# Kernel tuning notes

Measured on AMD Instinct MI355X. Metric: run time of the kernel, lower is better.

The kernel has to match this reference:

```python
import jax, jax.numpy as jnp
import numpy as np
from jax import lax

EPS = 1e-5
B = 512

def _conv(x, w, pad):
    # x: [B,Cin,H,W], w: [Cout,Cin,kh,kw]
    return lax.conv_general_dilated(x, w, (1, 1), [(pad, pad), (pad, pad)],
                                    dimension_numbers=('NCHW', 'OIHW', 'NCHW'))

def _bn2d(x, g, b, m, v):
    s = g * lax.rsqrt(v + EPS)
    return x * s[None, :, None, None] + (b - m * s)[None, :, None, None]

def _bn1d(x, g, b, m, v):
    s = g * lax.rsqrt(v + EPS)
    return x * s + (b - m * s)

def _pool2(x):
    return lax.reduce_window(x, -jnp.inf, lax.max, (1, 1, 2, 2), (1, 1, 2, 2), 'VALID')

def setup_inputs() -> dict:
    key = jax.random.key(0)
    ks = iter(jax.random.split(key, 64))
    rn = lambda shape, s=1.0: jax.random.normal(next(ks), shape, dtype=jnp.float32) * s
    un = lambda shape: jax.random.uniform(next(ks), shape, dtype=jnp.float32, minval=0.5, maxval=1.5)
    def bn_params(c):
        return (jnp.ones((c,), jnp.float32), jnp.zeros((c,), jnp.float32), rn((c,), 0.1), un((c,)))
    inp = {"x": rn((B, 3, 64, 64))}
    inp["w1"] = rn((32, 3, 5, 5), 0.1)
    inp["bn1_g"], inp["bn1_b"], inp["bn1_m"], inp["bn1_v"] = bn_params(32)
    inp["w2"] = rn((64, 32, 3, 3), 0.06)
    inp["bn2_g"], inp["bn2_b"], inp["bn2_m"], inp["bn2_v"] = bn_params(64)
    inp["w3"] = rn((128, 64, 3, 3), 0.04)
    inp["bn3_g"], inp["bn3_b"], inp["bn3_m"], inp["bn3_v"] = bn_params(128)
    inp["fc_w"] = rn((256, 8192), 0.01)
    inp["fc_b"] = jnp.zeros((256,), jnp.float32)
    inp["bnf_g"], inp["bnf_b"], inp["bnf_m"], inp["bnf_v"] = bn_params(256)
    inp["c_w1"] = rn((64, 256), 0.06)
    inp["c_b1"] = jnp.zeros((64,), jnp.float32)
    inp["bnc_g"], inp["bnc_b"], inp["bnc_m"], inp["bnc_v"] = bn_params(64)
    inp["c_w2"] = rn((1, 64), 0.1)
    inp["c_b2"] = jnp.zeros((1,), jnp.float32)
    inp["m_w1"] = rn((64, 256), 0.06)
    inp["m_b1"] = jnp.zeros((64,), jnp.float32)
    inp["bnm_g"], inp["bnm_b"], inp["bnm_m"], inp["bnm_v"] = bn_params(64)
    inp["m_w2"] = rn((1, 64), 0.1)
    inp["m_b2"] = jnp.zeros((1,), jnp.float32)
    return inp

def reference(x, w1, bn1_g, bn1_b, bn1_m, bn1_v,
              w2, bn2_g, bn2_b, bn2_m, bn2_v,
              w3, bn3_g, bn3_b, bn3_m, bn3_v,
              fc_w, fc_b, bnf_g, bnf_b, bnf_m, bnf_v,
              c_w1, c_b1, bnc_g, bnc_b, bnc_m, bnc_v, c_w2, c_b2,
              m_w1, m_b1, bnm_g, bnm_b, bnm_m, bnm_v, m_w2, m_b2):
    # Block 1: conv5x5(3->32) + BN + ReLU + maxpool2 -> [B,32,32,32]
    h = _pool2(jax.nn.relu(_bn2d(_conv(x, w1, 2), bn1_g, bn1_b, bn1_m, bn1_v)))
    # Block 2: conv3x3(32->64) + BN + ReLU + maxpool2 -> [B,64,16,16]
    h = _pool2(jax.nn.relu(_bn2d(_conv(h, w2, 1), bn2_g, bn2_b, bn2_m, bn2_v)))
    # Block 3: conv3x3(64->128) + BN + ReLU + maxpool2 + ToDense -> [B,128,8,8]
    h = _pool2(jax.nn.relu(_bn2d(_conv(h, w3, 1), bn3_g, bn3_b, bn3_m, bn3_v)))
    f = h.reshape(h.shape[0], -1)  # [B, 8192]
    s = jax.nn.relu(_bn1d(f @ fc_w.T + fc_b, bnf_g, bnf_b, bnf_m, bnf_v))  # [B,256]
    c = jax.nn.relu(_bn1d(s @ c_w1.T + c_b1, bnc_g, bnc_b, bnc_m, bnc_v)) @ c_w2.T + c_b2
    mo = jax.nn.relu(_bn1d(s @ m_w1.T + m_b1, bnm_g, bnm_b, bnm_m, bnm_v)) @ m_w2.T + m_b2
    return (c, mo)  # ([B,1], [B,1])
```

## Files before the change

### kernel.cpp

```cpp
#include <hip/hip_runtime.h>
#include <hip/hip_bf16.h>

#define EPS 1e-5f

typedef __attribute__((ext_vector_type(8))) short bf16x8;
typedef __attribute__((ext_vector_type(4))) float f32x4;

__device__ __forceinline__ ushort f2b(float f) {
    return __builtin_bit_cast(ushort, __float2bfloat16(f));
}
__device__ __forceinline__ bf16x8 ld_frag(const void* p) {
    return __builtin_bit_cast(bf16x8, *reinterpret_cast<const uint4*>(p));
}

__global__ __launch_bounds__(256) void k_prep_all(
    const float* __restrict__ w1, const float* __restrict__ w2,
    const float* __restrict__ w3, const float* __restrict__ fcw,
    const float* __restrict__ x,
    ushort* __restrict__ w1p, ushort* __restrict__ w2p, ushort* __restrict__ w3p,
    ushort* __restrict__ fcwp, ushort* __restrict__ x4p,
    ushort* __restrict__ h1p, ushort* __restrict__ h2p)
{
    __shared__ ushort l[128 * 66];
    const int bid = blockIdx.x, t = threadIdx.x;
    if (bid < 128) {
        const int total = 5120 + 18432 + 73728;
        for (int i = bid * 256 + t; i < total; i += 128 * 256) {
            if (i < 5120) {
                const int ky = i >> 10, co = (i >> 5) & 31, k = i & 31;
                const int kx = k >> 2, ci = k & 3;
                float v = 0.f;
                if (kx < 5 && ci < 3) v = w1[((co * 3 + ci) * 5 + ky) * 5 + kx];
                w1p[i] = f2b(v);
            } else if (i < 5120 + 18432) {
                const int j = i - 5120;
                const int tap = j >> 11, co = (j >> 5) & 63, ci = j & 31;
                w2p[j] = f2b(w2[(co * 32 + ci) * 9 + tap]);
            } else {
                const int j = i - (5120 + 18432);
                const int tap = j >> 13, co = (j >> 6) & 127, ci = j & 63;
                w3p[j] = f2b(w3[(co * 64 + ci) * 9 + tap]);
            }
        }
    } else if (bid < 384) {
        const int j = bid - 128;
        const float* src = fcw + (size_t)j * 8192;
        #pragma unroll
        for (int i = 0; i < 32; ++i) {
            const int idx = i * 256 + t;
            const int c = idx >> 6, p = idx & 63;
            l[c * 66 + p] = f2b(src[idx]);
        }
        __syncthreads();
        ushort* dst = fcwp + (size_t)j * 8192;
        #pragma unroll
        for (int i = 0; i < 32; ++i) {
            const int idx = i * 256 + t;
            const int c = idx & 127, p = idx >> 7;
            dst[idx] = l[c * 66 + p];
        }
    } else if (bid < 4480) {
        for (int p = (bid - 384) * 256 + t; p < 2506752; p += 4096 * 256) {
            const int n = p / 4896;
            const int rem = p - n * 4896;
            const int row = rem / 72, col = rem - row * 72;
            const int gr = row - 2, gc = col - 2;
            ushort4 pk; pk.x = 0; pk.y = 0; pk.z = 0; pk.w = 0;
            if ((unsigned)gr < 64u && (unsigned)gc < 64u) {
                const size_t base = ((size_t)n * 3 << 12) + (gr << 6) + gc;
                pk.x = f2b(x[base]); pk.y = f2b(x[base + 4096]); pk.z = f2b(x[base + 8192]);
            }
            *reinterpret_cast<ushort4*>(&x4p[(size_t)p * 4]) = pk;
        }
    } else if (bid < 4736) {
        const uint4 z = {0, 0, 0, 0};
        for (int i = (bid - 4480) * 256 + t; i < 270336; i += 256 * 256) {
            const int img = i / 528;
            const int rem = i - img * 528;
            const int px = rem >> 2, gg = rem & 3;
            int row, col;
            if (px < 34)      { row = 0;  col = px; }
            else if (px < 68) { row = 33; col = px - 34; }
            else { const int q = px - 68; row = 1 + (q >> 1); col = (q & 1) ? 33 : 0; }
            *reinterpret_cast<uint4*>(&h1p[(((size_t)img * 34 + row) * 34 + col) * 32 + gg * 8]) = z;
        }
    } else if (bid < 4992) {
        const uint4 z = {0, 0, 0, 0};
        for (int i = (bid - 4736) * 256 + t; i < 278528; i += 256 * 256) {
            const int img = i / 544;
            const int rem = i - img * 544;
            const int px = rem >> 3, gg = rem & 7;
            int row, col;
            if (px < 18)      { row = 0;  col = px; }
            else if (px < 36) { row = 17; col = px - 18; }
            else { const int q = px - 36; row = 1 + (q >> 1); col = (q & 1) ? 17 : 0; }
            *reinterpret_cast<uint4*>(&h2p[(((size_t)img * 18 + row) * 18 + col) * 64 + gg * 8]) = z;
        }
    }
}

__global__ __launch_bounds__(256) void k_conv1(
    const ushort* __restrict__ x4p, const ushort* __restrict__ w1p,
    const float* __restrict__ bg, const float* __restrict__ bb,
    const float* __restrict__ bm, const float* __restrict__ bv,
    ushort* __restrict__ h1p)
{
    __shared__ __align__(16) ushort xs[12 * 72 * 4];
    __shared__ __align__(16) ushort ws[5 * 32 * 32];
    const int bid = blockIdx.x;
    const int n = bid >> 3, q = bid & 7;
    const int t = threadIdx.x;
    const int wave = t >> 6, lane = t & 63;
    const int g = lane >> 4, l15 = lane & 15;

    {
        const ushort* src = x4p + ((size_t)(n * 68 + 8 * q) * 72) * 4;
        for (int i = t; i < 432; i += 256)
            *reinterpret_cast<uint4*>(&xs[i * 8]) = *reinterpret_cast<const uint4*>(src + i * 8);
    }
    for (int i = t; i < 640; i += 256) {
        const int gg = i & 3, r = i >> 2;
        const int co = r & 31;
        const uint4 v = *reinterpret_cast<const uint4*>(&w1p[r * 32 + gg * 8]);
        *reinterpret_cast<uint4*>((char*)ws + r * 64 + ((gg ^ ((co >> 1) & 3)) << 4)) = v;
    }
    __syncthreads();

    f32x4 acc[8][2];
    #pragma unroll
    for (int i = 0; i < 8; ++i) { acc[i][0] = (f32x4){0,0,0,0}; acc[i][1] = (f32x4){0,0,0,0}; }

    const char* xsb = (const char*)xs;
    const char* wsb = (const char*)ws;
    #pragma unroll
    for (int ky = 0; ky < 5; ++ky) {
        bf16x8 a[8], b[2];
        #pragma unroll
        for (int mt = 0; mt < 8; ++mt) {
            const int crl = 2 * wave + (mt >> 2);
            const int ccl = (mt & 3) * 16 + l15;
            const int off = ((crl + ky) * 72 + ccl) * 8 + g * 16;
            const uint2 lo = *reinterpret_cast<const uint2*>(xsb + off);
            const uint2 hi = *reinterpret_cast<const uint2*>(xsb + off + 8);
            uint4 all; all.x = lo.x; all.y = lo.y; all.z = hi.x; all.w = hi.y;
            a[mt] = __builtin_bit_cast(bf16x8, all);
        }
        #pragma unroll
        for (int nt = 0; nt < 2; ++nt) {
            const int co = nt * 16 + l15;
            b[nt] = ld_frag(wsb + (ky * 32 + co) * 64 + ((g ^ ((co >> 1) & 3)) << 4));
        }
        #pragma unroll
        for (int mt = 0; mt < 8; ++mt)
            #pragma unroll
            for (int nt = 0; nt < 2; ++nt)
                acc[mt][nt] = __builtin_amdgcn_mfma_f32_16x16x32_bf16(a[mt], b[nt], acc[mt][nt], 0, 0, 0);
    }

    const int prow = q * 4 + wave;
    #pragma unroll
    for (int nt = 0; nt < 2; ++nt) {
        const int co = nt * 16 + l15;
        const float s = bg[co] * rsqrtf(bv[co] + EPS);
        const float bsv = bb[co] - bm[co] * s;
        #pragma unroll
        for (int mt = 0; mt < 4; ++mt) {
            #pragma unroll
            for (int j = 0; j < 2; ++j) {
                const float v0 = fmaxf(fmaf(acc[mt][nt][2 * j],     s, bsv), 0.f);
                const float v1 = fmaxf(fmaf(acc[mt][nt][2 * j + 1], s, bsv), 0.f);
                const float v2 = fmaxf(fmaf(acc[mt + 4][nt][2 * j],     s, bsv), 0.f);
                const float v3 = fmaxf(fmaf(acc[mt + 4][nt][2 * j + 1], s, bsv), 0.f);
                const int ppc = mt * 8 + g * 2 + j;
                h1p[(((size_t)n * 34 + prow + 1) * 34 + ppc + 1) * 32 + co] =
                    f2b(fmaxf(fmaxf(v0, v1), fmaxf(v2, v3)));
            }
        }
    }
}

__global__ __launch_bounds__(256) void k_conv2(
    const ushort* __restrict__ h1p, const ushort* __restrict__ w2p,
    const float* __restrict__ bg, const float* __restrict__ bb,
    const float* __restrict__ bm, const float* __restrict__ bv,
    ushort* __restrict__ h2p)
{
    __shared__ __align__(16) ushort xs[10 * 34 * 32];
    __shared__ __align__(16) ushort ws[9 * 64 * 32];
    const int bid = blockIdx.x;
    const int n = bid >> 2, q = bid & 3;
    const int t = threadIdx.x;
    const int wave = t >> 6, lane = t & 63;
    const int g = lane >> 4, l15 = lane & 15;
    const char* xsb = (const char*)xs;
    const char* wsb = (const char*)ws;

    for (int i = t; i < 2304; i += 256) {
        const int gg = i & 3, r = i >> 2;
        const int co = r & 63;
        const uint4 v = *reinterpret_cast<const uint4*>(&w2p[r * 32 + gg * 8]);
        *reinterpret_cast<uint4*>((char*)ws + r * 64 + ((gg ^ ((co >> 1) & 3)) << 4)) = v;
    }
    {
        const ushort* src = h1p + ((size_t)(n * 34 + 8 * q) * 34) * 32;
        for (int i = t; i < 1360; i += 256) {
            const int gg = i & 3, pix = i >> 2;
            const uint4 v = *reinterpret_cast<const uint4*>(src + i * 8);
            *reinterpret_cast<uint4*>((char*)xs + pix * 64 + ((gg ^ ((pix >> 1) & 3)) << 4)) = v;
        }
    }
    __syncthreads();

    f32x4 acc[4][4];
    #pragma unroll
    for (int i = 0; i < 4; ++i)
        #pragma unroll
        for (int j = 0; j < 4; ++j) acc[i][j] = (f32x4){0,0,0,0};

    #pragma unroll
    for (int tap = 0; tap < 9; ++tap) {
        const int ky = tap / 3, kx = tap - 3 * ky;
        bf16x8 a[4], b[4];
        #pragma unroll
        for (int mt = 0; mt < 4; ++mt) {
            const int crl = 2 * wave + (mt >> 1);
            const int ccl = (mt & 1) * 16 + l15;
            const int pix = (crl + ky) * 34 + ccl + kx;
            a[mt] = ld_frag(xsb + pix * 64 + ((g ^ ((pix >> 1) & 3)) << 4));
        }
        #pragma unroll
        for (int nt = 0; nt < 4; ++nt) {
            const int co = nt * 16 + l15;
            b[nt] = ld_frag(wsb + (tap * 64 + co) * 64 + ((g ^ ((co >> 1) & 3)) << 4));
        }
        #pragma unroll
        for (int mt = 0; mt < 4; ++mt)
            #pragma unroll
            for (int nt = 0; nt < 4; ++nt)
                acc[mt][nt] = __builtin_amdgcn_mfma_f32_16x16x32_bf16(a[mt], b[nt], acc[mt][nt], 0, 0, 0);
    }

    const int prow = q * 4 + wave;
    #pragma unroll
    for (int nt = 0; nt < 4; ++nt) {
        const int co = nt * 16 + l15;
        const float s = bg[co] * rsqrtf(bv[co] + EPS);
        const float bsv = bb[co] - bm[co] * s;
        #pragma unroll
        for (int mtl = 0; mtl < 2; ++mtl) {
            #pragma unroll
            for (int j = 0; j < 2; ++j) {
                const float v0 = fmaxf(fmaf(acc[mtl][nt][2 * j],     s, bsv), 0.f);
                const float v1 = fmaxf(fmaf(acc[mtl][nt][2 * j + 1], s, bsv), 0.f);
                const float v2 = fmaxf(fmaf(acc[mtl + 2][nt][2 * j],     s, bsv), 0.f);
                const float v3 = fmaxf(fmaf(acc[mtl + 2][nt][2 * j + 1], s, bsv), 0.f);
                const int ppc = mtl * 8 + g * 2 + j;
                h2p[(((size_t)n * 18 + prow + 1) * 18 + ppc + 1) * 64 + co] =
                    f2b(fmaxf(fmaxf(v0, v1), fmaxf(v2, v3)));
            }
        }
    }
}

__global__ __launch_bounds__(256) void k_conv3(
    const ushort* __restrict__ h2p, const ushort* __restrict__ w3p,
    const float* __restrict__ bg, const float* __restrict__ bb,
    const float* __restrict__ bm, const float* __restrict__ bv,
    ushort* __restrict__ h3)
{
    __shared__ __align__(16) ushort xs[324 * 32];
    __shared__ __align__(16) ushort ws[9 * 64 * 32];
    const int bid = blockIdx.x;
    const int n = bid >> 1, ch = bid & 1;
    const int t = threadIdx.x;
    const int wave = t >> 6, lane = t & 63;
    const int g = lane >> 4, l15 = lane & 15;
    const char* xsb = (const char*)xs;
    const char* wsb = (const char*)ws;

    f32x4 acc[4][4];
    #pragma unroll
    for (int i = 0; i < 4; ++i)
        #pragma unroll
        for (int j = 0; j < 4; ++j) acc[i][j] = (f32x4){0,0,0,0};

    for (int gci = 0; gci < 2; ++gci) {
        if (gci) __syncthreads();
        for (int i = t; i < 1296; i += 256) {
            const int gg = i & 3, pix = i >> 2;
            const uint4 v = *reinterpret_cast<const uint4*>(
                &h2p[((size_t)n * 324 + pix) * 64 + gci * 32 + gg * 8]);
            *reinterpret_cast<uint4*>((char*)xs + pix * 64 + ((gg ^ ((pix >> 1) & 3)) << 4)) = v;
        }
        for (int i = t; i < 2304; i += 256) {
            const int gg = i & 3, r = i >> 2;
            const int tap = r >> 6, co = r & 63;
            const uint4 v = *reinterpret_cast<const uint4*>(
                &w3p[((size_t)(tap * 128 + ch * 64 + co) << 6) + gci * 32 + gg * 8]);
            *reinterpret_cast<uint4*>((char*)ws + r * 64 + ((gg ^ ((co >> 1) & 3)) << 4)) = v;
        }
        __syncthreads();
        #pragma unroll
        for (int tap = 0; tap < 9; ++tap) {
            const int ky = tap / 3, kx = tap - 3 * ky;
            bf16x8 a[4], b[4];
            #pragma unroll
            for (int mt = 0; mt < 4; ++mt) {
                const int pr = 4 * wave + mt;
                const int pix = (pr + ky) * 18 + l15 + kx;
                a[mt] = ld_frag(xsb + pix * 64 + ((g ^ ((pix >> 1) & 3)) << 4));
            }
            #pragma unroll
            for (int nt = 0; nt < 4; ++nt) {
                const int co = nt * 16 + l15;
                b[nt] = ld_frag(wsb + (tap * 64 + co) * 64 + ((g ^ ((co >> 1) & 3)) << 4));
            }
            #pragma unroll
            for (int mt = 0; mt < 4; ++mt)
                #pragma unroll
                for (int nt = 0; nt < 4; ++nt)
                    acc[mt][nt] = __builtin_amdgcn_mfma_f32_16x16x32_bf16(a[mt], b[nt], acc[mt][nt], 0, 0, 0);
        }
    }

    #pragma unroll
    for (int nt = 0; nt < 4; ++nt) {
        const int co = ch * 64 + nt * 16 + l15;
        const float s = bg[co] * rsqrtf(bv[co] + EPS);
        const float bsv = bb[co] - bm[co] * s;
        #pragma unroll
        for (int mtl = 0; mtl < 2; ++mtl) {
            #pragma unroll
            for (int j = 0; j < 2; ++j) {
                const int mt = mtl * 2;
                const float v0 = fmaxf(fmaf(acc[mt][nt][2 * j],     s, bsv), 0.f);
                const float v1 = fmaxf(fmaf(acc[mt][nt][2 * j + 1], s, bsv), 0.f);
                const float v2 = fmaxf(fmaf(acc[mt + 1][nt][2 * j],     s, bsv), 0.f);
                const float v3 = fmaxf(fmaf(acc[mt + 1][nt][2 * j + 1], s, bsv), 0.f);
                const int ppr = 2 * wave + mtl;
                const int pcol = g * 2 + j;
                h3[(((size_t)n * 8 + ppr) * 8 + pcol) * 128 + co] =
                    f2b(fmaxf(fmaxf(v0, v1), fmaxf(v2, v3)));
            }
        }
    }
}

__global__ __launch_bounds__(256) void k_fc(
    const ushort* __restrict__ A, const ushort* __restrict__ Bw, float* __restrict__ C)
{
    __shared__ __align__(16) ushort As[64 * 32];
    __shared__ __align__(16) ushort Bs[64 * 32];
    const int bm = blockIdx.x, bn = blockIdx.y, kz = blockIdx.z;
    const int t = threadIdx.x;
    const int wave = t >> 6, lane = t & 63;
    const int g = lane >> 4, l15 = lane & 15;

    f32x4 acc[4];
    #pragma unroll
    for (int i = 0; i < 4; ++i) acc[i] = (f32x4){0,0,0,0};

    const char* asb = (const char*)As;
    const char* bsb = (const char*)Bs;
    for (int kk = 0; kk < 16; ++kk) {
        const int k0 = kz * 512 + kk * 32;
        if (kk) __syncthreads();
        {
            const int gg = t & 3, row = t >> 2;
            const uint4 va = *reinterpret_cast<const uint4*>(
                &A[(size_t)(bm * 64 + row) * 8192 + k0 + gg * 8]);
            *reinterpret_cast<uint4*>((char*)As + row * 64 + ((gg ^ ((row >> 1) & 3)) << 4)) = va;
            const uint4 vb = *reinterpret_cast<const uint4*>(
                &Bw[(size_t)(bn * 64 + row) * 8192 + k0 + gg * 8]);
            *reinterpret_cast<uint4*>((char*)Bs + row * 64 + ((gg ^ ((row >> 1) & 3)) << 4)) = vb;
        }
        __syncthreads();
        bf16x8 a[4], b;
        #pragma unroll
        for (int mt = 0; mt < 4; ++mt) {
            const int r = mt * 16 + l15;
            a[mt] = ld_frag(asb + r * 64 + ((g ^ ((r >> 1) & 3)) << 4));
        }
        {
            const int r = wave * 16 + l15;
            b = ld_frag(bsb + r * 64 + ((g ^ ((r >> 1) & 3)) << 4));
        }
        #pragma unroll
        for (int mt = 0; mt < 4; ++mt)
            acc[mt] = __builtin_amdgcn_mfma_f32_16x16x32_bf16(a[mt], b, acc[mt], 0, 0, 0);
    }

    float* Cp = C + (size_t)kz * 512 * 256;
    const int col = bn * 64 + wave * 16 + l15;
    #pragma unroll
    for (int mt = 0; mt < 4; ++mt) {
        #pragma unroll
        for (int r = 0; r < 4; ++r) {
            const int row = bm * 64 + mt * 16 + g * 4 + r;
            Cp[(size_t)row * 256 + col] = acc[mt][r];
        }
    }
}

__global__ __launch_bounds__(128) void k_heads(
    const float* __restrict__ sraw, const float* __restrict__ fcb,
    const float* __restrict__ fg, const float* __restrict__ fb,
    const float* __restrict__ fm, const float* __restrict__ fv,
    const float* __restrict__ cw1, const float* __restrict__ cb1,
    const float* __restrict__ cg, const float* __restrict__ cbb,
    const float* __restrict__ cm, const float* __restrict__ cv,
    const float* __restrict__ cw2, const float* __restrict__ cb2,
    const float* __restrict__ mw1, const float* __restrict__ mb1,
    const float* __restrict__ mg, const float* __restrict__ mbb,
    const float* __restrict__ mm, const float* __restrict__ mv,
    const float* __restrict__ mw2, const float* __restrict__ mb2,
    float* __restrict__ outp)
{
    __shared__ float sv[256];
    const int b = blockIdx.x, t = threadIdx.x;
    for (int k = t; k < 256; k += 128) {
        float val = fcb[k];
        #pragma unroll
        for (int z = 0; z < 16; ++z) val += sraw[(size_t)z * 131072 + b * 256 + k];
        const float s = fg[k] * rsqrtf(fv[k] + EPS);
        sv[k] = fmaxf(fmaf(val, s, fb[k] - fm[k] * s), 0.f);
    }
    __syncthreads();
    const int j = t & 63;
    const bool isM = (t >= 64);
    const float* w1  = isM ? mw1 : cw1;
    const float* b1  = isM ? mb1 : cb1;
    const float* g1  = isM ? mg  : cg;
    const float* bb1 = isM ? mbb : cbb;
    const float* m1  = isM ? mm  : cm;
    const float* v1  = isM ? mv  : cv;
    const float* w2  = isM ? mw2 : cw2;
    const float* b2  = isM ? mb2 : cb2;
    float d = 0.f;
    const float* wr = w1 + j * 256;
    #pragma unroll 8
    for (int k = 0; k < 256; ++k) d = fmaf(sv[k], wr[k], d);
    d += b1[j];
    const float s1 = g1[j] * rsqrtf(v1[j] + EPS);
    d = fmaxf(fmaf(d, s1, bb1[j] - m1[j] * s1), 0.f);
    float prod = d * w2[j];
    #pragma unroll
    for (int off = 32; off > 0; off >>= 1) prod += __shfl_down(prod, off);
    if (j == 0) outp[(isM ? 512 : 0) + b] = prod + b2[0];
}

extern "C" void kernel_launch(void* const* d_in, const int* in_sizes, int n_in,
                              void* d_out, int out_size, void* d_ws, size_t ws_size,
                              hipStream_t stream)
{
    const float* x    = (const float*)d_in[0];
    const float* w1   = (const float*)d_in[1];
    const float* bn1g = (const float*)d_in[2];
    const float* bn1b = (const float*)d_in[3];
    const float* bn1m = (const float*)d_in[4];
    const float* bn1v = (const float*)d_in[5];
    const float* w2   = (const float*)d_in[6];
    const float* bn2g = (const float*)d_in[7];
    const float* bn2b = (const float*)d_in[8];
    const float* bn2m = (const float*)d_in[9];
    const float* bn2v = (const float*)d_in[10];
    const float* w3   = (const float*)d_in[11];
    const float* bn3g = (const float*)d_in[12];
    const float* bn3b = (const float*)d_in[13];
    const float* bn3m = (const float*)d_in[14];
    const float* bn3v = (const float*)d_in[15];
    const float* fcw  = (const float*)d_in[16];
    const float* fcb  = (const float*)d_in[17];
    const float* bnfg = (const float*)d_in[18];
    const float* bnfb = (const float*)d_in[19];
    const float* bnfm = (const float*)d_in[20];
    const float* bnfv = (const float*)d_in[21];
    const float* cw1  = (const float*)d_in[22];
    const float* cb1  = (const float*)d_in[23];
    const float* bncg = (const float*)d_in[24];
    const float* bncb = (const float*)d_in[25];
    const float* bncm = (const float*)d_in[26];
    const float* bncv = (const float*)d_in[27];
    const float* cw2  = (const float*)d_in[28];
    const float* cb2  = (const float*)d_in[29];
    const float* mw1  = (const float*)d_in[30];
    const float* mb1  = (const float*)d_in[31];
    const float* bnmg = (const float*)d_in[32];
    const float* bnmb = (const float*)d_in[33];
    const float* bnmm = (const float*)d_in[34];
    const float* bnmv = (const float*)d_in[35];
    const float* mw2  = (const float*)d_in[36];
    const float* mb2  = (const float*)d_in[37];

    char* W = (char*)d_ws;
    ushort* x4p  = (ushort*)(W);
    ushort* h1p  = (ushort*)(W + 20054016);
    ushort* h2p  = (ushort*)(W + 57933824);
    ushort* h3   = (ushort*)(W + 79167488);
    ushort* w1p  = (ushort*)(W + 87556096);
    ushort* w2p  = (ushort*)(W + 87566336);
    ushort* w3p  = (ushort*)(W + 87603200);
    ushort* fcwp = (ushort*)(W + 87750656);
    float*  sr   = (float*) (W + 91944960);
    float* outp = (float*)d_out;

    k_prep_all<<<4992, 256, 0, stream>>>(w1, w2, w3, fcw, x,
                                         w1p, w2p, w3p, fcwp, x4p, h1p, h2p);
    k_conv1<<<512 * 8, 256, 0, stream>>>(x4p, w1p, bn1g, bn1b, bn1m, bn1v, h1p);
    k_conv2<<<512 * 4, 256, 0, stream>>>(h1p, w2p, bn2g, bn2b, bn2m, bn2v, h2p);
    k_conv3<<<512 * 2, 256, 0, stream>>>(h2p, w3p, bn3g, bn3b, bn3m, bn3v, h3);
    k_fc<<<dim3(8, 4, 16), 256, 0, stream>>>(h3, fcwp, sr);
    k_heads<<<512, 128, 0, stream>>>(sr, fcb, bnfg, bnfb, bnfm, bnfv,
                                     cw1, cb1, bncg, bncb, bncm, bncv, cw2, cb2,
                                     mw1, mb1, bnmg, bnmb, bnmm, bnmv, mw2, mb2, outp);
}
```

Baseline: 250.0 us.

## Fold BN scale into conv weights and read weights from global instead of LDS

The BN scale for conv1-3 is now multiplied into the bf16 weights in the prep kernel, and the per-channel bias is precomputed into small workspace buffers, so the epilogues only do add+ReLU. The conv kernels no longer stage weights into shared memory; B fragments are loaded straight from global memory, which is expected to hit in L1/L2. This removes the weight-staging stores and lowers LDS use, and launch_bounds(256,4) asks for higher occupancy. The cost is uncoalesced or repeated global loads inside the MFMA loop, and scaling before the bf16 rounding changes the numerics slightly.

```diff
diff --git a/kernel.cpp b/kernel.cpp
--- a/kernel.cpp
+++ b/kernel.cpp
@@ -17,13 +17,34 @@
     const float* __restrict__ w1, const float* __restrict__ w2,
     const float* __restrict__ w3, const float* __restrict__ fcw,
     const float* __restrict__ x,
+    const float* __restrict__ bn1g, const float* __restrict__ bn1b,
+    const float* __restrict__ bn1m, const float* __restrict__ bn1v,
+    const float* __restrict__ bn2g, const float* __restrict__ bn2b,
+    const float* __restrict__ bn2m, const float* __restrict__ bn2v,
+    const float* __restrict__ bn3g, const float* __restrict__ bn3b,
+    const float* __restrict__ bn3m, const float* __restrict__ bn3v,
     ushort* __restrict__ w1p, ushort* __restrict__ w2p, ushort* __restrict__ w3p,
+    float* __restrict__ b1f, float* __restrict__ b2f, float* __restrict__ b3f,
     ushort* __restrict__ fcwp, ushort* __restrict__ x4p,
     ushort* __restrict__ h1p, ushort* __restrict__ h2p)
 {
     __shared__ ushort l[128 * 66];
     const int bid = blockIdx.x, t = threadIdx.x;
     if (bid < 128) {
+        if (bid == 0 && t < 224) {
+            if (t < 32) {
+                const float s = bn1g[t] * rsqrtf(bn1v[t] + EPS);
+                b1f[t] = bn1b[t] - bn1m[t] * s;
+            } else if (t < 96) {
+                const int c = t - 32;
+                const float s = bn2g[c] * rsqrtf(bn2v[c] + EPS);
+                b2f[c] = bn2b[c] - bn2m[c] * s;
+            } else {
+                const int c = t - 96;
+                const float s = bn3g[c] * rsqrtf(bn3v[c] + EPS);
+                b3f[c] = bn3b[c] - bn3m[c] * s;
+            }
+        }
         const int total = 5120 + 18432 + 73728;
         for (int i = bid * 256 + t; i < total; i += 128 * 256) {
             if (i < 5120) {
@@ -31,15 +52,18 @@
                 const int kx = k >> 2, ci = k & 3;
                 float v = 0.f;
                 if (kx < 5 && ci < 3) v = w1[((co * 3 + ci) * 5 + ky) * 5 + kx];
-                w1p[i] = f2b(v);
+                const float s = bn1g[co] * rsqrtf(bn1v[co] + EPS);
+                w1p[i] = f2b(v * s);
             } else if (i < 5120 + 18432) {
                 const int j = i - 5120;
                 const int tap = j >> 11, co = (j >> 5) & 63, ci = j & 31;
-                w2p[j] = f2b(w2[(co * 32 + ci) * 9 + tap]);
+                const float s = bn2g[co] * rsqrtf(bn2v[co] + EPS);
+                w2p[j] = f2b(w2[(co * 32 + ci) * 9 + tap] * s);
             } else {
                 const int j = i - (5120 + 18432);
                 const int tap = j >> 13, co = (j >> 6) & 127, ci = j & 63;
-                w3p[j] = f2b(w3[(co * 64 + ci) * 9 + tap]);
+                const float s = bn3g[co] * rsqrtf(bn3v[co] + EPS);
+                w3p[j] = f2b(w3[(co * 64 + ci) * 9 + tap] * s);
             }
         }
     } else if (bid < 384) {
@@ -99,14 +123,11 @@
     }
 }
 
-__global__ __launch_bounds__(256) void k_conv1(
+__global__ __launch_bounds__(256, 4) void k_conv1(
     const ushort* __restrict__ x4p, const ushort* __restrict__ w1p,
-    const float* __restrict__ bg, const float* __restrict__ bb,
-    const float* __restrict__ bm, const float* __restrict__ bv,
-    ushort* __restrict__ h1p)
+    const float* __restrict__ bias, ushort* __restrict__ h1p)
 {
     __shared__ __align__(16) ushort xs[12 * 72 * 4];
-    __shared__ __align__(16) ushort ws[5 * 32 * 32];
     const int bid = blockIdx.x;
     const int n = bid >> 3, q = bid & 7;
     const int t = threadIdx.x;
@@ -118,12 +139,6 @@
         for (int i = t; i < 432; i += 256)
             *reinterpret_cast<uint4*>(&xs[i * 8]) = *reinterpret_cast<const uint4*>(src + i * 8);
     }
-    for (int i = t; i < 640; i += 256) {
-        const int gg = i & 3, r = i >> 2;
-        const int co = r & 31;
-        const uint4 v = *reinterpret_cast<const uint4*>(&w1p[r * 32 + gg * 8]);
-        *reinterpret_cast<uint4*>((char*)ws + r * 64 + ((gg ^ ((co >> 1) & 3)) << 4)) = v;
-    }
     __syncthreads();
 
     f32x4 acc[8][2];
@@ -131,7 +146,6 @@
     for (int i = 0; i < 8; ++i) { acc[i][0] = (f32x4){0,0,0,0}; acc[i][1] = (f32x4){0,0,0,0}; }
 
     const char* xsb = (const char*)xs;
-    const char* wsb = (const char*)ws;
     #pragma unroll
     for (int ky = 0; ky < 5; ++ky) {
         bf16x8 a[8], b[2];
@@ -148,7 +162,7 @@
         #pragma unroll
         for (int nt = 0; nt < 2; ++nt) {
             const int co = nt * 16 + l15;
-            b[nt] = ld_frag(wsb + (ky * 32 + co) * 64 + ((g ^ ((co >> 1) & 3)) << 4));
+            b[nt] = ld_frag(&w1p[(ky * 32 + co) * 32 + g * 8]);
         }
         #pragma unroll
         for (int mt = 0; mt < 8; ++mt)
@@ -161,16 +175,15 @@
     #pragma unroll
     for (int nt = 0; nt < 2; ++nt) {
         const int co = nt * 16 + l15;
-        const float s = bg[co] * rsqrtf(bv[co] + EPS);
-        const float bsv = bb[co] - bm[co] * s;
+        const float bsv = bias[co];
         #pragma unroll
         for (int mt = 0; mt < 4; ++mt) {
             #pragma unroll
             for (int j = 0; j < 2; ++j) {
-                const float v0 = fmaxf(fmaf(acc[mt][nt][2 * j],     s, bsv), 0.f);
-                const float v1 = fmaxf(fmaf(acc[mt][nt][2 * j + 1], s, bsv), 0.f);
-                const float v2 = fmaxf(fmaf(acc[mt + 4][nt][2 * j],     s, bsv), 0.f);
-                const float v3 = fmaxf(fmaf(acc[mt + 4][nt][2 * j + 1], s, bsv), 0.f);
+                const float v0 = fmaxf(acc[mt][nt][2 * j]     + bsv, 0.f);
+                const float v1 = fmaxf(acc[mt][nt][2 * j + 1] + bsv, 0.f);
+                const float v2 = fmaxf(acc[mt + 4][nt][2 * j]     + bsv, 0.f);
+                const float v3 = fmaxf(acc[mt + 4][nt][2 * j + 1] + bsv, 0.f);
                 const int ppc = mt * 8 + g * 2 + j;
                 h1p[(((size_t)n * 34 + prow + 1) * 34 + ppc + 1) * 32 + co] =
                     f2b(fmaxf(fmaxf(v0, v1), fmaxf(v2, v3)));
@@ -179,28 +192,18 @@
     }
 }
 
-__global__ __launch_bounds__(256) void k_conv2(
+__global__ __launch_bounds__(256, 4) void k_conv2(
     const ushort* __restrict__ h1p, const ushort* __restrict__ w2p,
-    const float* __restrict__ bg, const float* __restrict__ bb,
-    const float* __restrict__ bm, const float* __restrict__ bv,
-    ushort* __restrict__ h2p)
+    const float* __restrict__ bias, ushort* __restrict__ h2p)
 {
     __shared__ __align__(16) ushort xs[10 * 34 * 32];
-    __shared__ __align__(16) ushort ws[9 * 64 * 32];
     const int bid = blockIdx.x;
     const int n = bid >> 2, q = bid & 3;
     const int t = threadIdx.x;
     const int wave = t >> 6, lane = t & 63;
     const int g = lane >> 4, l15 = lane & 15;
     const char* xsb = (const char*)xs;
-    const char* wsb = (const char*)ws;
-
-    for (int i = t; i < 2304; i += 256) {
-        const int gg = i & 3, r = i >> 2;
-        const int co = r & 63;
-        const uint4 v = *reinterpret_cast<const uint4*>(&w2p[r * 32 + gg * 8]);
-        *reinterpret_cast<uint4*>((char*)ws + r * 64 + ((gg ^ ((co >> 1) & 3)) << 4)) = v;
-    }
+
     {
         const ushort* src = h1p + ((size_t)(n * 34 + 8 * q) * 34) * 32;
         for (int i = t; i < 1360; i += 256) {
@@ -231,7 +234,7 @@
         #pragma unroll
         for (int nt = 0; nt < 4; ++nt) {
             const int co = nt * 16 + l15;
-            b[nt] = ld_frag(wsb + (tap * 64 + co) * 64 + ((g ^ ((co >> 1) & 3)) << 4));
+            b[nt] = ld_frag(&w2p[(tap * 64 + co) * 32 + g * 8]);
         }
         #pragma unroll
         for (int mt = 0; mt < 4; ++mt)
@@ -244,16 +247,15 @@
     #pragma unroll
     for (int nt = 0; nt < 4; ++nt) {
         const int co = nt * 16 + l15;
-        const float s = bg[co] * rsqrtf(bv[co] + EPS);
-        const float bsv = bb[co] - bm[co] * s;
+        const float bsv = bias[co];
         #pragma unroll
         for (int mtl = 0; mtl < 2; ++mtl) {
             #pragma unroll
             for (int j = 0; j < 2; ++j) {
-                const float v0 = fmaxf(fmaf(acc[mtl][nt][2 * j],     s, bsv), 0.f);
-                const float v1 = fmaxf(fmaf(acc[mtl][nt][2 * j + 1], s, bsv), 0.f);
-                const float v2 = fmaxf(fmaf(acc[mtl + 2][nt][2 * j],     s, bsv), 0.f);
-                const float v3 = fmaxf(fmaf(acc[mtl + 2][nt][2 * j + 1], s, bsv), 0.f);
+                const float v0 = fmaxf(acc[mtl][nt][2 * j]     + bsv, 0.f);
+                const float v1 = fmaxf(acc[mtl][nt][2 * j + 1] + bsv, 0.f);
+                const float v2 = fmaxf(acc[mtl + 2][nt][2 * j]     + bsv, 0.f);
+                const float v3 = fmaxf(acc[mtl + 2][nt][2 * j + 1] + bsv, 0.f);
                 const int ppc = mtl * 8 + g * 2 + j;
                 h2p[(((size_t)n * 18 + prow + 1) * 18 + ppc + 1) * 64 + co] =
                     f2b(fmaxf(fmaxf(v0, v1), fmaxf(v2, v3)));
@@ -262,21 +264,17 @@
     }
 }
 
-__global__ __launch_bounds__(256) void k_conv3(
+__global__ __launch_bounds__(256, 4) void k_conv3(
     const ushort* __restrict__ h2p, const ushort* __restrict__ w3p,
-    const float* __restrict__ bg, const float* __restrict__ bb,
-    const float* __restrict__ bm, const float* __restrict__ bv,
-    ushort* __restrict__ h3)
+    const float* __restrict__ bias, ushort* __restrict__ h3)
 {
     __shared__ __align__(16) ushort xs[324 * 32];
-    __shared__ __align__(16) ushort ws[9 * 64 * 32];
     const int bid = blockIdx.x;
     const int n = bid >> 1, ch = bid & 1;
     const int t = threadIdx.x;
     const int wave = t >> 6, lane = t & 63;
     const int g = lane >> 4, l15 = lane & 15;
     const char* xsb = (const char*)xs;
-    const char* wsb = (const char*)ws;
 
     f32x4 acc[4][4];
     #pragma unroll
@@ -292,13 +290,6 @@
                 &h2p[((size_t)n * 324 + pix) * 64 + gci * 32 + gg * 8]);
             *reinterpret_cast<uint4*>((char*)xs + pix * 64 + ((gg ^ ((pix >> 1) & 3)) << 4)) = v;
         }
-        for (int i = t; i < 2304; i += 256) {
-            const int gg = i & 3, r = i >> 2;
-            const int tap = r >> 6, co = r & 63;
-            const uint4 v = *reinterpret_cast<const uint4*>(
-                &w3p[((size_t)(tap * 128 + ch * 64 + co) << 6) + gci * 32 + gg * 8]);
-            *reinterpret_cast<uint4*>((char*)ws + r * 64 + ((gg ^ ((co >> 1) & 3)) << 4)) = v;
-        }
         __syncthreads();
         #pragma unroll
         for (int tap = 0; tap < 9; ++tap) {
@@ -312,8 +303,8 @@
             }
             #pragma unroll
             for (int nt = 0; nt < 4; ++nt) {
-                const int co = nt * 16 + l15;
-                b[nt] = ld_frag(wsb + (tap * 64 + co) * 64 + ((g ^ ((co >> 1) & 3)) << 4));
+                const int co = ch * 64 + nt * 16 + l15;
+                b[nt] = ld_frag(&w3p[((size_t)(tap * 128 + co)) * 64 + gci * 32 + g * 8]);
             }
             #pragma unroll
             for (int mt = 0; mt < 4; ++mt)
@@ -326,17 +317,16 @@
     #pragma unroll
     for (int nt = 0; nt < 4; ++nt) {
         const int co = ch * 64 + nt * 16 + l15;
-        const float s = bg[co] * rsqrtf(bv[co] + EPS);
-        const float bsv = bb[co] - bm[co] * s;
+        const float bsv = bias[co];
         #pragma unroll
         for (int mtl = 0; mtl < 2; ++mtl) {
             #pragma unroll
             for (int j = 0; j < 2; ++j) {
                 const int mt = mtl * 2;
-                const float v0 = fmaxf(fmaf(acc[mt][nt][2 * j],     s, bsv), 0.f);
-                const float v1 = fmaxf(fmaf(acc[mt][nt][2 * j + 1], s, bsv), 0.f);
-                const float v2 = fmaxf(fmaf(acc[mt + 1][nt][2 * j],     s, bsv), 0.f);
-                const float v3 = fmaxf(fmaf(acc[mt + 1][nt][2 * j + 1], s, bsv), 0.f);
+                const float v0 = fmaxf(acc[mt][nt][2 * j]     + bsv, 0.f);
+                const float v1 = fmaxf(acc[mt][nt][2 * j + 1] + bsv, 0.f);
+                const float v2 = fmaxf(acc[mt + 1][nt][2 * j]     + bsv, 0.f);
+                const float v3 = fmaxf(acc[mt + 1][nt][2 * j + 1] + bsv, 0.f);
                 const int ppr = 2 * wave + mtl;
                 const int pcol = g * 2 + j;
                 h3[(((size_t)n * 8 + ppr) * 8 + pcol) * 128 + co] =
@@ -501,14 +491,21 @@
     ushort* w2p  = (ushort*)(W + 87566336);
     ushort* w3p  = (ushort*)(W + 87603200);
     ushort* fcwp = (ushort*)(W + 87750656);
-    float*  sr   = (float*) (W + 91944960);
+    float*  b1f  = (float*) (W + 91944960);
+    float*  b2f  = (float*) (W + 91945088);
+    float*  b3f  = (float*) (W + 91945344);
+    float*  sr   = (float*) (W + 91946496);
     float* outp = (float*)d_out;
 
     k_prep_all<<<4992, 256, 0, stream>>>(w1, w2, w3, fcw, x,
-                                         w1p, w2p, w3p, fcwp, x4p, h1p, h2p);
-    k_conv1<<<512 * 8, 256, 0, stream>>>(x4p, w1p, bn1g, bn1b, bn1m, bn1v, h1p);
-    k_conv2<<<512 * 4, 256, 0, stream>>>(h1p, w2p, bn2g, bn2b, bn2m, bn2v, h2p);
-    k_conv3<<<512 * 2, 256, 0, stream>>>(h2p, w3p, bn3g, bn3b, bn3m, bn3v, h3);
+                                         bn1g, bn1b, bn1m, bn1v,
+                                         bn2g, bn2b, bn2m, bn2v,
+                                         bn3g, bn3b, bn3m, bn3v,
+                                         w1p, w2p, w3p, b1f, b2f, b3f,
+                                         fcwp, x4p, h1p, h2p);
+    k_conv1<<<512 * 8, 256, 0, stream>>>(x4p, w1p, b1f, h1p);
+    k_conv2<<<512 * 4, 256, 0, stream>>>(h1p, w2p, b2f, h2p);
+    k_conv3<<<512 * 2, 256, 0, stream>>>(h2p, w3p, b3f, h3);
     k_fc<<<dim3(8, 4, 16), 256, 0, stream>>>(h3, fcwp, sr);
     k_heads<<<512, 128, 0, stream>>>(sr, fcb, bnfg, bnfb, bnfm, bnfv,
                                      cw1, cb1, bncg, bncb, bncm, bncv, cw2, cb2,
```

After: 285.0 us. 14.0% more time.
